# Performance work log

Hardware: AMD Instinct MI355X
Metric: run time of the kernel (lower is better)

The kernel has to match this reference:

```python
import jax, jax.numpy as jnp
import numpy as np

B, D, O, E, K = 8192, 2048, 2048, 8, 2


def setup_inputs() -> dict:
    key = jax.random.key(0)
    k1, k2, k3, k4 = jax.random.split(key, 4)
    x = jax.random.normal(k1, (B, D), dtype=jnp.float32)
    # router: Linear(D -> E)
    router_w = jax.random.normal(k2, (E, D), dtype=jnp.float32) * (1.0 / np.sqrt(D))
    router_b = jnp.zeros((E,), dtype=jnp.float32)
    # experts: [E, O, D] weight (xavier-uniform-like scale), [E, O] bias (zeros)
    lim = np.sqrt(6.0 / (D + O))
    expert_w = jax.random.uniform(k3, (E, O, D), dtype=jnp.float32, minval=-lim, maxval=lim)
    expert_b = jnp.zeros((E, O), dtype=jnp.float32)
    return {"x": x, "router_w": router_w, "router_b": router_b,
            "expert_w": expert_w, "expert_b": expert_b}


def reference(x, router_w, router_b, expert_w, expert_b):
    # router logits [B, E]
    logits = x @ router_w.T + router_b
    top_vals, top_idx = jax.lax.top_k(logits, K)          # [B, K]
    routing_weights = jax.nn.softmax(top_vals, axis=-1)   # softmax over top-k logits
    # dense per-(token, expert) combine weight [B, E]; zero for unselected experts
    onehot = jax.nn.one_hot(top_idx, E, dtype=x.dtype)    # [B, K, E]
    w_be = jnp.einsum('bk,bke->be', routing_weights, onehot)
    # per-expert linear, weighted combine (loop over small fixed E)
    out = jnp.zeros((x.shape[0], O), dtype=x.dtype)
    for e in range(E):
        out = out + w_be[:, e:e + 1] * (x @ expert_w[e].T + expert_b[e])
    return out
```

## Files before the change

### kernel.cpp

```cpp
#include <hip/hip_runtime.h>
#include <stdint.h>

#define NB 8192
#define ND 2048
#define NO 2048
#define NE 8
#define BK 64
#define NT (ND / BK)
#define BM 256
#define BN 256
#define MAXW 40

typedef __bf16 bf16x8 __attribute__((ext_vector_type(8)));
typedef float floatx4 __attribute__((ext_vector_type(4)));

__device__ __forceinline__ unsigned short f2bf(float f) {
    union { float f; uint32_t u; } v; v.f = f;
    uint32_t u = v.u;
    return (unsigned short)((u + 0x7FFFu + ((u >> 16) & 1u)) >> 16);
}

__global__ __launch_bounds__(256) void cvt_kernel(
        const float* __restrict__ w, unsigned short* __restrict__ ob) {
    const int n4W = NE * NO * ND / 4;
    int i = blockIdx.x * blockDim.x + threadIdx.x;
    int stride = gridDim.x * blockDim.x;
    for (; i < n4W; i += stride) {
        float4 v = ((const float4*)w)[i];
        ushort4 o;
        o.x = f2bf(v.x); o.y = f2bf(v.y); o.z = f2bf(v.z); o.w = f2bf(v.w);
        ((ushort4*)ob)[i] = o;
    }
}

__global__ __launch_bounds__(256) void router_topk_kernel(const float* __restrict__ x,
        const float* __restrict__ rw, const float* __restrict__ rb,
        unsigned short* __restrict__ xbf,
        int* __restrict__ i0a, int* __restrict__ i1a,
        float* __restrict__ w0a, float* __restrict__ w1a,
        int* __restrict__ cnt) {
    if (blockIdx.x == 0 && threadIdx.x < 2 * NE) cnt[threadIdx.x] = 0;
    const int wave = threadIdx.x >> 6;
    const int lane = threadIdx.x & 63;
    const int t = blockIdx.x * 4 + wave;
    const float4* xp = (const float4*)(x + (size_t)t * ND);
    const float4* rp = (const float4*)rw;
    ushort4* xo = (ushort4*)(xbf + (size_t)t * ND);
    float acc[NE];
#pragma unroll
    for (int e = 0; e < NE; e++) acc[e] = 0.f;
#pragma unroll
    for (int i = 0; i < ND / 256; i++) {
        int idx = i * 64 + lane;
        float4 xv = xp[idx];
        ushort4 o;
        o.x = f2bf(xv.x); o.y = f2bf(xv.y); o.z = f2bf(xv.z); o.w = f2bf(xv.w);
        xo[idx] = o;
#pragma unroll
        for (int e = 0; e < NE; e++) {
            float4 rv = rp[(size_t)e * (ND / 4) + idx];
            acc[e] += xv.x * rv.x + xv.y * rv.y + xv.z * rv.z + xv.w * rv.w;
        }
    }
#pragma unroll
    for (int e = 0; e < NE; e++) {
        float v = acc[e];
#pragma unroll
        for (int s = 32; s > 0; s >>= 1) v += __shfl_xor(v, s, 64);
        acc[e] = v;
    }
    if (lane == 0) {
        float lg[NE];
#pragma unroll
        for (int e = 0; e < NE; e++) lg[e] = acc[e] + rb[e];
        int i0 = 0; float v0 = lg[0];
#pragma unroll
        for (int e = 1; e < NE; e++) if (lg[e] > v0) { v0 = lg[e]; i0 = e; }
        int i1 = -1; float v1 = -3.4e38f;
#pragma unroll
        for (int e = 0; e < NE; e++) if (e != i0 && lg[e] > v1) { v1 = lg[e]; i1 = e; }
        float ex = expf(v1 - v0);
        float inv = 1.f / (1.f + ex);
        i0a[t] = i0; i1a[t] = i1;
        w0a[t] = inv; w1a[t] = ex * inv;
    }
}

__global__ __launch_bounds__(256) void compact_kernel(
        const int* __restrict__ i0a, const int* __restrict__ i1a,
        const float* __restrict__ w0a, const float* __restrict__ w1a,
        int* __restrict__ cntA, int* __restrict__ cntB,
        int* __restrict__ tokA, float* __restrict__ wA,
        int* __restrict__ tokB, float* __restrict__ wB) {
    const int lane = threadIdx.x & 63;
    const int gw = (blockIdx.x * 256 + threadIdx.x) >> 6;
    const int t = gw * 64 + lane;
#pragma unroll
    for (int which = 0; which < 2; which++) {
        int sel   = which ? i1a[t] : i0a[t];
        float w   = which ? w1a[t] : w0a[t];
        int* cnt  = which ? cntB : cntA;
        int* tok  = which ? tokB : tokA;
        float* wl = which ? wB : wA;
        unsigned long long m[NE];
#pragma unroll
        for (int e = 0; e < NE; e++) m[e] = __ballot(sel == e);
        int slot = __popcll(m[sel] & ((1ull << lane) - 1ull));
        int base = 0;
        if (lane < NE) base = atomicAdd(&cnt[lane], (int)__popcll(m[lane]));
        base = __shfl(base, sel, 64);
        tok[sel * NB + base + slot] = t;
        wl[sel * NB + base + slot]  = w;
    }
}

#define GLL16(g, l) __builtin_amdgcn_global_load_lds( \
    (const __attribute__((address_space(1))) void*)(g), \
    (__attribute__((address_space(3))) void*)(l), 16, 0, 0)

#define BAR __builtin_amdgcn_s_barrier()
#define WAITL asm volatile("s_waitcnt lgkmcnt(0)" ::: "memory")

#define LDA(HALFPTR) do {                                                   \
    const char* _p = (const char*)(HALFPTR);                                \
    _Pragma("unroll") for (int mi = 0; mi < 4; mi++)                        \
        _Pragma("unroll") for (int kk = 0; kk < 2; kk++)                    \
            af[mi][kk] = *(const bf16x8*)(_p + offA[mi][kk]);               \
} while (0)

#define LDB(HALFPTR) do {                                                   \
    const char* _p = (const char*)(HALFPTR);                                \
    _Pragma("unroll") for (int nj = 0; nj < 2; nj++)                        \
        _Pragma("unroll") for (int kk = 0; kk < 2; kk++)                    \
            bfr[nj][kk] = *(const bf16x8*)(_p + offB[nj][kk]);              \
} while (0)

#define MMAC(MH, NH) do {                                                   \
    __builtin_amdgcn_s_setprio(1);                                          \
    _Pragma("unroll") for (int kk = 0; kk < 2; kk++)                        \
        _Pragma("unroll") for (int mi = 0; mi < 4; mi++)                    \
            _Pragma("unroll") for (int nj = 0; nj < 2; nj++)                \
                acc[(MH)*4+mi][(NH)*2+nj] =                                 \
                    __builtin_amdgcn_mfma_f32_16x16x32_bf16(                \
                        af[mi][kk], bfr[nj][kk],                            \
                        acc[(MH)*4+mi][(NH)*2+nj], 0, 0, 0);                \
    __builtin_amdgcn_s_setprio(0);                                          \
} while (0)

#define STG_A(D, H, KT) do { if ((KT) < NT) {                               \
    GLL16(bA[H][0] + (size_t)(KT) * 128, (char*)sA[D][H] + tid * 16);       \
    GLL16(bA[H][1] + (size_t)(KT) * 128, (char*)sA[D][H] + 8192 + tid * 16);\
} } while (0)
#define STG_B(D, H, KT) do { if ((KT) < NT) {                               \
    GLL16(bB[H][0] + (size_t)(KT) * 128, (char*)sB[D][H] + tid * 16);       \
    GLL16(bB[H][1] + (size_t)(KT) * 128, (char*)sB[D][H] + 8192 + tid * 16);\
} } while (0)

template <bool ACCUM>
__global__ __launch_bounds__(512, 2) void moe_gemm_kernel(
        const unsigned short* __restrict__ xbf, const unsigned short* __restrict__ wbf,
        const float* __restrict__ eb, const int* __restrict__ cntArr,
        const int* __restrict__ listTok, const float* __restrict__ listW,
        float* __restrict__ out) {
    __shared__ unsigned short sA[2][2][128 * 64];
    __shared__ unsigned short sB[2][2][128 * 64];

    const int bid = blockIdx.x;
    const int nt = bid & 7;
    const int widx = bid >> 3;
    int e = 0, mt = 0;
    {
        int acc0 = 0; int found = 0;
#pragma unroll
        for (int k = 0; k < NE; k++) {
            int nmt = (cntArr[k] + BM - 1) >> 8;
            if (!found && widx < acc0 + nmt) { e = k; mt = widx - acc0; found = 1; }
            acc0 += nmt;
        }
        if (!found) return;
    }
    const int cnt = cntArr[e];
    const int tid = threadIdx.x;

    const int prow0 = tid >> 3;
    const int prow1 = 64 + (tid >> 3);
    const int scol  = ((tid & 7) * 16) ^ (((tid >> 3) & 7) << 4);
    const char* bA[2][2]; const char* bB[2][2];
#pragma unroll
    for (int h = 0; h < 2; h++) {
        int g0 = mt * BM + h * 128 + prow0;
        int g1 = mt * BM + h * 128 + prow1;
        int tk0 = (g0 < cnt) ? listTok[e * NB + g0] : 0;
        int tk1 = (g1 < cnt) ? listTok[e * NB + g1] : 0;
        bA[h][0] = (const char*)xbf + (size_t)tk0 * (ND * 2) + scol;
        bA[h][1] = (const char*)xbf + (size_t)tk1 * (ND * 2) + scol;
        bB[h][0] = (const char*)wbf + ((size_t)e * NO + (size_t)nt * BN + h * 128 + prow0) * (ND * 2) + scol;
        bB[h][1] = (const char*)wbf + ((size_t)e * NO + (size_t)nt * BN + h * 128 + prow1) * (ND * 2) + scol;
    }

    const int wave = tid >> 6, lane = tid & 63;
    const int wm2 = wave >> 2;
    const int wn2 = wave & 3;
    const int lr = lane & 15, lq = lane >> 4;
    const int xorv = (lr & 7) << 4;
    int offA[4][2], offB[2][2];
#pragma unroll
    for (int mi = 0; mi < 4; mi++)
#pragma unroll
        for (int kk = 0; kk < 2; kk++)
            offA[mi][kk] = (wm2 * 64 + mi * 16 + lr) * 128 + ((kk * 64 + lq * 16) ^ xorv);
#pragma unroll
    for (int nj = 0; nj < 2; nj++)
#pragma unroll
        for (int kk = 0; kk < 2; kk++)
            offB[nj][kk] = (wn2 * 32 + nj * 16 + lr) * 128 + ((kk * 64 + lq * 16) ^ xorv);

    bf16x8 af[4][2], bfr[2][2];
    floatx4 acc[8][4];
#pragma unroll
    for (int i = 0; i < 8; i++)
#pragma unroll
        for (int j = 0; j < 4; j++) acc[i][j] = (floatx4){0.f, 0.f, 0.f, 0.f};

    STG_A(0, 0, 0); STG_A(0, 1, 0); STG_B(0, 0, 0); STG_B(0, 1, 0);
    STG_A(1, 0, 1); STG_A(1, 1, 1); STG_B(1, 1, 1);
    asm volatile("s_waitcnt vmcnt(6)" ::: "memory");
    BAR;

#pragma unroll 1
    for (int i = 0; i < NT / 2; i++) {
        const int t1 = 2 * i + 1, t2 = 2 * i + 2, t3 = 2 * i + 3;
        LDA(sA[0][0]); LDB(sB[0][0]);
        STG_B(1, 0, t1);
        BAR; MMAC(0, 0); WAITL; BAR;
        LDB(sB[0][1]);
        STG_A(0, 0, t2);
        BAR; MMAC(0, 1); WAITL; BAR;
        LDA(sA[0][1]);
        STG_B(0, 1, t2);
        BAR; MMAC(1, 1); WAITL; BAR;
        LDB(sB[0][0]);
        STG_A(0, 1, t2);
        BAR; MMAC(1, 0); WAITL;
        if (t2 < NT) { asm volatile("s_waitcnt vmcnt(6)" ::: "memory"); }
        else         { asm volatile("s_waitcnt vmcnt(0)" ::: "memory"); }
        BAR;
        LDA(sA[1][0]); LDB(sB[1][0]);
        STG_B(0, 0, t2);
        BAR; MMAC(0, 0); WAITL; BAR;
        LDB(sB[1][1]);
        STG_A(1, 0, t3);
        BAR; MMAC(0, 1); WAITL; BAR;
        LDA(sA[1][1]);
        STG_B(1, 1, t3);
        BAR; MMAC(1, 1); WAITL; BAR;
        LDB(sB[1][0]);
        STG_A(1, 1, t3);
        BAR; MMAC(1, 0); WAITL;
        if (t3 < NT) { asm volatile("s_waitcnt vmcnt(6)" ::: "memory"); }
        else         { asm volatile("s_waitcnt vmcnt(0)" ::: "memory"); }
        BAR;
    }

    float ebv[4];
#pragma unroll
    for (int nh = 0; nh < 2; nh++)
#pragma unroll
        for (int nj = 0; nj < 2; nj++)
            ebv[nh * 2 + nj] = eb[(size_t)e * NO + nt * BN + nh * 128 + wn2 * 32 + nj * 16 + lr];
#pragma unroll
    for (int mh = 0; mh < 2; mh++)
#pragma unroll
    for (int mi = 0; mi < 4; mi++)
#pragma unroll
    for (int r = 0; r < 4; r++) {
        int gr = mt * BM + mh * 128 + wm2 * 64 + mi * 16 + lq * 4 + r;
        if (gr < cnt) {
            int tk   = listTok[e * NB + gr];
            float wg = listW[e * NB + gr];
            float* op = out + (size_t)tk * NO + nt * BN + lr;
#pragma unroll
            for (int nh = 0; nh < 2; nh++)
#pragma unroll
            for (int nj = 0; nj < 2; nj++) {
                float* p = op + nh * 128 + wn2 * 32 + nj * 16;
                float v = wg * (acc[mh * 4 + mi][nh * 2 + nj][r] + ebv[nh * 2 + nj]);
                if (ACCUM) v += *p;
                *p = v;
            }
        }
    }
}

extern "C" void kernel_launch(void* const* d_in, const int* in_sizes, int n_in,
                              void* d_out, int out_size, void* d_ws, size_t ws_size,
                              hipStream_t stream) {
    const float* x        = (const float*)d_in[0];
    const float* router_w = (const float*)d_in[1];
    const float* router_b = (const float*)d_in[2];
    const float* expert_w = (const float*)d_in[3];
    const float* expert_b = (const float*)d_in[4];
    float* out = (float*)d_out;
    char* ws = (char*)d_ws;

    unsigned short* xbf = (unsigned short*)ws;
    unsigned short* wbf = (unsigned short*)(ws + 33554432);
    size_t o = 100663296;
    int*   tokA = (int*)(ws + o);   o += NE * NB * 4;
    float* wA   = (float*)(ws + o); o += NE * NB * 4;
    int*   tokB = (int*)(ws + o);   o += NE * NB * 4;
    float* wB   = (float*)(ws + o); o += NE * NB * 4;
    int*   i0a  = (int*)(ws + o);   o += NB * 4;
    int*   i1a  = (int*)(ws + o);   o += NB * 4;
    float* w0a  = (float*)(ws + o); o += NB * 4;
    float* w1a  = (float*)(ws + o); o += NB * 4;
    int*   cnt  = (int*)(ws + o);   o += 128;
    int* cntA = cnt;
    int* cntB = cnt + 8;

    router_topk_kernel<<<NB / 4, 256, 0, stream>>>(x, router_w, router_b, xbf,
                                                   i0a, i1a, w0a, w1a, cnt);
    cvt_kernel<<<2048, 256, 0, stream>>>(expert_w, wbf);
    compact_kernel<<<NB / 64 / 4, 256, 0, stream>>>(i0a, i1a, w0a, w1a,
                                                    cntA, cntB, tokA, wA, tokB, wB);
    moe_gemm_kernel<false><<<MAXW * 8, 512, 0, stream>>>(
        xbf, wbf, expert_b, cntA, tokA, wA, out);
    moe_gemm_kernel<true><<<MAXW * 8, 512, 0, stream>>>(
        xbf, wbf, expert_b, cntB, tokB, wB, out);
}
```

Baseline: 553.2 us.

## Fuse router and weight conversion; use fixed expert-interleaved GEMM grid with early exit

Merges the router/top-k kernel and the expert-weight bf16 conversion into one launch, with extra blocks doing the conversion. This removes a launch boundary and lets the two memory-bound phases overlap. The MoE GEMM grid no longer walks the per-expert counts with a prefix scan to find its tile. Each block now derives expert, N-tile and M-tile directly from its block index over a fixed 2048-block grid and returns early if its tile is empty. That drops the serial scan but launches many idle blocks and changes the tile ordering, which affects L2 reuse of expert weights.

```diff
diff --git a/kernel.cpp b/kernel.cpp
--- a/kernel.cpp
+++ b/kernel.cpp
@@ -9,7 +9,6 @@
 #define NT (ND / BK)
 #define BM 256
 #define BN 256
-#define MAXW 40
 
 typedef __bf16 bf16x8 __attribute__((ext_vector_type(8)));
 typedef float floatx4 __attribute__((ext_vector_type(4)));
@@ -20,25 +19,25 @@
     return (unsigned short)((u + 0x7FFFu + ((u >> 16) & 1u)) >> 16);
 }
 
-__global__ __launch_bounds__(256) void cvt_kernel(
-        const float* __restrict__ w, unsigned short* __restrict__ ob) {
-    const int n4W = NE * NO * ND / 4;
-    int i = blockIdx.x * blockDim.x + threadIdx.x;
-    int stride = gridDim.x * blockDim.x;
-    for (; i < n4W; i += stride) {
-        float4 v = ((const float4*)w)[i];
-        ushort4 o;
-        o.x = f2bf(v.x); o.y = f2bf(v.y); o.z = f2bf(v.z); o.w = f2bf(v.w);
-        ((ushort4*)ob)[i] = o;
-    }
-}
-
-__global__ __launch_bounds__(256) void router_topk_kernel(const float* __restrict__ x,
+__global__ __launch_bounds__(256) void router_cvt_kernel(const float* __restrict__ x,
         const float* __restrict__ rw, const float* __restrict__ rb,
         unsigned short* __restrict__ xbf,
+        const float* __restrict__ ew, unsigned short* __restrict__ wbf,
         int* __restrict__ i0a, int* __restrict__ i1a,
         float* __restrict__ w0a, float* __restrict__ w1a,
         int* __restrict__ cnt) {
+    if (blockIdx.x >= NB / 4) {
+        const int n4W = NE * NO * ND / 4;
+        int i = (blockIdx.x - NB / 4) * 256 + threadIdx.x;
+        const int stride = 2048 * 256;
+        for (; i < n4W; i += stride) {
+            float4 v = ((const float4*)ew)[i];
+            ushort4 o;
+            o.x = f2bf(v.x); o.y = f2bf(v.y); o.z = f2bf(v.z); o.w = f2bf(v.w);
+            ((ushort4*)wbf)[i] = o;
+        }
+        return;
+    }
     if (blockIdx.x == 0 && threadIdx.x < 2 * NE) cnt[threadIdx.x] = 0;
     const int wave = threadIdx.x >> 6;
     const int lane = threadIdx.x & 63;
@@ -166,20 +165,12 @@
     __shared__ unsigned short sB[2][2][128 * 64];
 
     const int bid = blockIdx.x;
-    const int nt = bid & 7;
-    const int widx = bid >> 3;
-    int e = 0, mt = 0;
-    {
-        int acc0 = 0; int found = 0;
-#pragma unroll
-        for (int k = 0; k < NE; k++) {
-            int nmt = (cntArr[k] + BM - 1) >> 8;
-            if (!found && widx < acc0 + nmt) { e = k; mt = widx - acc0; found = 1; }
-            acc0 += nmt;
-        }
-        if (!found) return;
-    }
+    const int e = bid & 7;
+    const int j = bid >> 3;
+    const int nt = j & 7;
+    const int mt = j >> 3;
     const int cnt = cntArr[e];
+    if (mt * BM >= cnt) return;
     const int tid = threadIdx.x;
 
     const int prow0 = tid >> 3;
@@ -220,7 +211,7 @@
 #pragma unroll
     for (int i = 0; i < 8; i++)
 #pragma unroll
-        for (int j = 0; j < 4; j++) acc[i][j] = (floatx4){0.f, 0.f, 0.f, 0.f};
+        for (int j2 = 0; j2 < 4; j2++) acc[i][j2] = (floatx4){0.f, 0.f, 0.f, 0.f};
 
     STG_A(0, 0, 0); STG_A(0, 1, 0); STG_B(0, 0, 0); STG_B(0, 1, 0);
     STG_A(1, 0, 1); STG_A(1, 1, 1); STG_B(1, 1, 1);
@@ -318,13 +309,12 @@
     int* cntA = cnt;
     int* cntB = cnt + 8;
 
-    router_topk_kernel<<<NB / 4, 256, 0, stream>>>(x, router_w, router_b, xbf,
-                                                   i0a, i1a, w0a, w1a, cnt);
-    cvt_kernel<<<2048, 256, 0, stream>>>(expert_w, wbf);
+    router_cvt_kernel<<<NB / 4 + 2048, 256, 0, stream>>>(
+        x, router_w, router_b, xbf, expert_w, wbf, i0a, i1a, w0a, w1a, cnt);
     compact_kernel<<<NB / 64 / 4, 256, 0, stream>>>(i0a, i1a, w0a, w1a,
                                                     cntA, cntB, tokA, wA, tokB, wB);
-    moe_gemm_kernel<false><<<MAXW * 8, 512, 0, stream>>>(
+    moe_gemm_kernel<false><<<2048, 512, 0, stream>>>(
         xbf, wbf, expert_b, cntA, tokA, wA, out);
-    moe_gemm_kernel<true><<<MAXW * 8, 512, 0, stream>>>(
+    moe_gemm_kernel<true><<<2048, 512, 0, stream>>>(
         xbf, wbf, expert_b, cntB, tokB, wB, out);
 }
```

Result: faster. 541.6 us (-2.1%).
